# Kernel tuning notes

Hardware: AMD Instinct MI355X
Metric: run time of the kernel (lower is better)

## Reference

```python
import jax, jax.numpy as jnp
import numpy as np

B, N, D = 8, 4096, 512
NUM_CODES = 8192

def setup_inputs() -> dict:
    key = jax.random.key(0)
    kx, kc = jax.random.split(key)
    x = jax.random.normal(kx, (B, N, D), dtype=jnp.float32)
    codebook = jax.random.normal(kc, (NUM_CODES, D), dtype=jnp.float32)
    return {"x": x, "codebook": codebook}

def reference(x, codebook):
    # x: (B, N, D); codebook: (K, D)
    b = x.shape[0]
    flat = x.reshape(-1, x.shape[-1])  # (B*N, D)
    distances = (
        jnp.sum(flat * flat, axis=1, keepdims=True)
        + jnp.sum(codebook * codebook, axis=1)
        - 2.0 * flat @ codebook.T
    )
    codes = jnp.argmin(distances, axis=1).reshape(b, -1)  # (B, N) int
    return codes
```

## Files before the change

### kernel.cpp

```cpp
#include <hip/hip_runtime.h>
#include <hip/hip_bf16.h>
#include <hip/hip_fp16.h>


#define M_ROWS 32768
#define DDIM   512
#define KCODES 8192
#define NCAND  8

typedef unsigned long long u64;
typedef unsigned int u32;
typedef __attribute__((ext_vector_type(4))) float f32x4;
typedef __attribute__((ext_vector_type(2))) long l64x2;

#define GL2LDS(gp, lp) __builtin_amdgcn_global_load_lds(                  \
    (const __attribute__((address_space(1))) void*)(gp),                  \
    (__attribute__((address_space(3))) void*)(lp), 16, 0, 0)

__device__ __forceinline__ u32 umin32(u32 a, u32 b) { return a < b ? a : b; }
__device__ __forceinline__ u32 umax32(u32 a, u32 b) { return a > b ? a : b; }
__device__ __forceinline__ u64 umin64(u64 a, u64 b) { return a < b ? a : b; }

__device__ __forceinline__ u32 fsort(float s) {
  u32 fb = __float_as_uint(s);
  return fb ^ (u32)(((int)fb >> 31) | 0x80000000);
}

__device__ __forceinline__ uint2 pk8_fp8(float4 v0, float4 v1) {
  int lo = 0, hi = 0;
  lo = __builtin_amdgcn_cvt_pk_fp8_f32(v0.x, v0.y, lo, false);
  lo = __builtin_amdgcn_cvt_pk_fp8_f32(v0.z, v0.w, lo, true);
  hi = __builtin_amdgcn_cvt_pk_fp8_f32(v1.x, v1.y, hi, false);
  hi = __builtin_amdgcn_cvt_pk_fp8_f32(v1.z, v1.w, hi, true);
  return (uint2){(u32)lo, (u32)hi};
}

__device__ __forceinline__ size_t frag_addr(int row, int lane8 ) {
  const int c  = lane8 >> 4;
  const int k16 = lane8 & 15;
  const int ks = k16 >> 2;
  const int g  = k16 & 3;
  const int q  = g * 2 + (ks >> 1);
  const int slot = q ^ (row & 7);
  return (size_t)row * 512 + c * 128 + slot * 16 + (ks & 1) * 8;
}

__global__ __launch_bounds__(256) void conv_codebook_kernel(
    const float* __restrict__ cb, unsigned char* __restrict__ ch8,
    float* __restrict__ cnh) {
  int wave = (blockIdx.x * 256 + threadIdx.x) >> 6;
  int lane = threadIdx.x & 63;
  if (wave >= KCODES) return;
  const float* src = cb + (size_t)wave * DDIM + lane * 8;
  float4 v0 = *(const float4*)(src);
  float4 v1 = *(const float4*)(src + 4);
  *(uint2*)(ch8 + frag_addr(wave, lane)) = pk8_fp8(v0, v1);
  float ss = v0.x*v0.x + v0.y*v0.y + v0.z*v0.z + v0.w*v0.w
           + v1.x*v1.x + v1.y*v1.y + v1.z*v1.z + v1.w*v1.w;
#pragma unroll
  for (int off = 32; off; off >>= 1) ss += __shfl_xor(ss, off);
  if (lane == 0) cnh[wave] = 0.5f * ss;
}

__global__ __launch_bounds__(256) void conv_x_kernel(
    const float* __restrict__ x, unsigned char* __restrict__ xh8) {
  int wave = (blockIdx.x * 256 + threadIdx.x) >> 6;
  int lane = threadIdx.x & 63;
  const float* src = x + (size_t)wave * DDIM + lane * 8;
  float4 v0 = *(const float4*)(src);
  float4 v1 = *(const float4*)(src + 4);
  *(uint2*)(xh8 + frag_addr(wave, lane)) = pk8_fp8(v0, v1);
}

__global__ __launch_bounds__(256) void coarse_kernel(
    const unsigned char* __restrict__ xh8, const unsigned char* __restrict__ ch8,
    const float* __restrict__ cnh, uint4* __restrict__ part) {
  __shared__ __align__(16) char smem[34816];
  char* aL = smem;
  char* bL = smem + 16384;
  uint4* tab = (uint4*)smem;

  const int tid  = threadIdx.x;
  const int lane = tid & 63;
  const int wid  = tid >> 6;
  const int wm   = wid >> 1, wn = wid & 1;
  const int g    = lane >> 4, l16 = lane & 15;

  const int mblk = blockIdx.x & 255;
  const int nblk = blockIdx.x >> 8;
  const int row0 = mblk * 128;
  const int col0 = nblk * 128;

  const int a_ = lane >> 3, b_ = lane & 7;
  const int slot0 = (g * 2) ^ (l16 & 7);

  f32x4 acc[4][4];
#pragma unroll
  for (int tm = 0; tm < 4; ++tm)
#pragma unroll
    for (int tn = 0; tn < 4; ++tn) acc[tm][tn] = (f32x4){0.f, 0.f, 0.f, 0.f};

  for (int c = 0; c < 4; ++c) {
    __syncthreads();
#pragma unroll
    for (int j = 0; j < 4; ++j) {
      const int I = wid * 4 + j;
      const size_t srcoff = (size_t)(I * 8 + a_) * 512 + c * 128 + b_ * 16;
      GL2LDS(xh8 + (size_t)row0 * 512 + srcoff, aL + I * 1024);
      GL2LDS(ch8 + (size_t)col0 * 512 + srcoff, bL + I * 1024);
    }
    __syncthreads();
#pragma unroll
    for (int ks2 = 0; ks2 < 2; ++ks2) {
      const int slot = slot0 ^ ks2;
      l64x2 af[4], bf[4];
#pragma unroll
      for (int t = 0; t < 4; ++t) {
        const int ra = wm * 64 + t * 16 + l16;
        const int rb = wn * 64 + t * 16 + l16;
        af[t] = *(const l64x2*)&aL[ra * 128 + slot * 16];
        bf[t] = *(const l64x2*)&bL[rb * 128 + slot * 16];
      }
#pragma unroll
      for (int h = 0; h < 2; ++h)
#pragma unroll
        for (int tm = 0; tm < 4; ++tm)
#pragma unroll
          for (int tn = 0; tn < 4; ++tn)
            acc[tm][tn] = __builtin_amdgcn_mfma_f32_16x16x32_fp8_fp8(
                af[tm][h], bf[tn][h], acc[tm][tn], 0, 0, 0);
    }
  }

  u32 codev[4];
  float cn[4];
#pragma unroll
  for (int tn = 0; tn < 4; ++tn) {
    codev[tn] = (u32)(col0 + wn * 64 + tn * 16 + l16);
    cn[tn] = cnh[codev[tn]];
  }

  u32 k1[16], k2[16], k3[16];
#pragma unroll
  for (int tm = 0; tm < 4; ++tm)
#pragma unroll
    for (int r = 0; r < 4; ++r) {
      const int sl = tm * 4 + r;
      k1[sl] = ~0u; k2[sl] = ~0u; k3[sl] = ~0u;
#pragma unroll
      for (int tn = 0; tn < 4; ++tn) {
        float s = cn[tn] - acc[tm][tn][r];
        u32 key = (__float_as_uint(s) & 0xFFFFE000u) | codev[tn];
        u32 t1 = umax32(k1[sl], key); k1[sl] = umin32(k1[sl], key);
        u32 t2 = umax32(k2[sl], t1);  k2[sl] = umin32(k2[sl], t1);
        k3[sl] = umin32(k3[sl], t2);
      }
    }

  u32 m1 = ~0u, m2 = ~0u, m3 = ~0u;
#pragma unroll
  for (int p = 0; p < 2; ++p) {
    __syncthreads();
    if (wn == p) {
#pragma unroll
      for (int tm = 0; tm < 4; ++tm)
#pragma unroll
        for (int r = 0; r < 4; ++r) {
          const int row = wm * 64 + tm * 16 + g * 4 + r;
          const int sl = tm * 4 + r;
          tab[row * 17 + l16] = (uint4){k1[sl], k2[sl], k3[sl], 0u};
        }
    }
    __syncthreads();
    if (tid < 128) {
#pragma unroll
      for (int e = 0; e < 16; ++e) {
        uint4 v = tab[tid * 17 + e];
        u32 t1 = umax32(m1, v.x); m1 = umin32(m1, v.x);
        u32 t2 = umax32(m2, t1);  m2 = umin32(m2, t1);
        m3 = umin32(m3, t2);
        t1 = umax32(m2, v.y);     m2 = umin32(m2, v.y);
        m3 = umin32(m3, t1);
        m3 = umin32(m3, v.z);
      }
    }
  }

  if (tid < 128)
    part[(size_t)nblk * M_ROWS + row0 + tid] = (uint4){m1, m2, m3, 0u};
}

__global__ __launch_bounds__(256) void merge_kernel(
    const uint4* __restrict__ part, int* __restrict__ cand) {
  const int row = blockIdx.x * 256 + threadIdx.x;
  u32 k[NCAND];
#pragma unroll
  for (int i = 0; i < NCAND; ++i) k[i] = ~0u;
  for (int nb = 0; nb < KCODES / 128; ++nb) {
    uint4 e = part[(size_t)nb * M_ROWS + row];
    u32 t = e.x;
#pragma unroll
    for (int i = 0; i < NCAND; ++i) { u32 mx = umax32(k[i], t); k[i] = umin32(k[i], t); t = mx; }
    t = e.y;
#pragma unroll
    for (int i = 0; i < NCAND; ++i) { u32 mx = umax32(k[i], t); k[i] = umin32(k[i], t); t = mx; }
    t = e.z;
#pragma unroll
    for (int i = 0; i < NCAND; ++i) { u32 mx = umax32(k[i], t); k[i] = umin32(k[i], t); t = mx; }
  }
#pragma unroll
  for (int i = 0; i < NCAND; ++i)
    cand[row * NCAND + i] = (int)(k[i] & 0x1FFFu);
}

__global__ __launch_bounds__(256) void rescore_kernel(
    const float* __restrict__ x, const float* __restrict__ cb,
    const float* __restrict__ cnh, const int* __restrict__ cand,
    int* __restrict__ out) {
  int wave = (blockIdx.x * 256 + threadIdx.x) >> 6;
  int lane = threadIdx.x & 63;
  if (wave >= M_ROWS) return;
  int idx[NCAND];
#pragma unroll
  for (int j = 0; j < NCAND; ++j) idx[j] = cand[wave * NCAND + j];

  const float* xr = x + (size_t)wave * DDIM + lane * 8;
  float4 x0 = *(const float4*)(xr);
  float4 x1 = *(const float4*)(xr + 4);

  float d[NCAND];
#pragma unroll
  for (int j = 0; j < NCAND; ++j) {
    const float* c = cb + (size_t)idx[j] * DDIM + lane * 8;
    float4 a0 = *(const float4*)(c);
    float4 a1 = *(const float4*)(c + 4);
    d[j] = x0.x*a0.x + x0.y*a0.y + x0.z*a0.z + x0.w*a0.w
         + x1.x*a1.x + x1.y*a1.y + x1.z*a1.z + x1.w*a1.w;
  }
#pragma unroll
  for (int off = 32; off; off >>= 1)
#pragma unroll
    for (int j = 0; j < NCAND; ++j) d[j] += __shfl_xor(d[j], off);

  if (lane == 0) {
    u64 best = ~0ull;
#pragma unroll
    for (int j = 0; j < NCAND; ++j) {
      float s = cnh[idx[j]] - d[j];
      u64 key = ((u64)fsort(s) << 32) | (u32)idx[j];
      best = umin64(best, key);
    }
    out[wave] = (int)(u32)best;
  }
}

extern "C" void kernel_launch(void* const* d_in, const int* in_sizes, int n_in,
                              void* d_out, int out_size, void* d_ws, size_t ws_size,
                              hipStream_t stream) {
  const float* x  = (const float*)d_in[0];
  const float* cb = (const float*)d_in[1];
  int* out = (int*)d_out;

  char* ws = (char*)d_ws;
  unsigned char* ch8  = (unsigned char*)(ws);
  unsigned char* xh8  = (unsigned char*)(ws + (size_t)4 * 1024 * 1024);
  float*         cnh  = (float*)(ws + (size_t)20 * 1024 * 1024);
  int*           cand = (int*)(ws + (size_t)20 * 1024 * 1024 + 32 * 1024);
  uint4*         part = (uint4*)(ws + (size_t)21 * 1024 * 1024);

  conv_codebook_kernel<<<KCODES / 4, 256, 0, stream>>>(cb, ch8, cnh);
  conv_x_kernel<<<M_ROWS / 4, 256, 0, stream>>>(x, xh8);
  coarse_kernel<<<(M_ROWS / 128) * (KCODES / 128), 256, 0, stream>>>(xh8, ch8, cnh, part);
  merge_kernel<<<M_ROWS / 256, 256, 0, stream>>>(part, cand);
  rescore_kernel<<<M_ROWS / 4, 256, 0, stream>>>(x, cb, cnh, cand, out);
}
```

Measured before the change: 403.3 us.

## Switch coarse GEMM to gfx950 16x16x128 scaled FP8 MFMA with row-major layout

Replaces the 16x16x32 FP8 MFMA sequence with the gfx950 mfma_scale 16x16x128 f8f6f4 instruction using unit scales (0x7F), so each K-chunk of 128 takes one MFMA per tile instead of four. The FP8 conversion kernels now write plain row-major data, and the XOR swizzle moves into the global-to-LDS copy addresses. Fragments are read from LDS as two 16-byte pieces per lane. The part buffer offset is also moved. The risk is that the new fragment K-ordering must match for both A and B, which is fine for a dot product, and the wider operands raise register pressure.

Result: faster. 383.5 us (-4.9%).

```diff
diff --git a/kernel.cpp b/kernel.cpp
--- a/kernel.cpp
+++ b/kernel.cpp
@@ -11,7 +11,7 @@
 typedef unsigned long long u64;
 typedef unsigned int u32;
 typedef __attribute__((ext_vector_type(4))) float f32x4;
-typedef __attribute__((ext_vector_type(2))) long l64x2;
+typedef __attribute__((ext_vector_type(8))) int v8i;
 
 #define GL2LDS(gp, lp) __builtin_amdgcn_global_load_lds(                  \
     (const __attribute__((address_space(1))) void*)(gp),                  \
@@ -33,16 +33,6 @@
   hi = __builtin_amdgcn_cvt_pk_fp8_f32(v1.x, v1.y, hi, false);
   hi = __builtin_amdgcn_cvt_pk_fp8_f32(v1.z, v1.w, hi, true);
   return (uint2){(u32)lo, (u32)hi};
-}
-
-__device__ __forceinline__ size_t frag_addr(int row, int lane8 ) {
-  const int c  = lane8 >> 4;
-  const int k16 = lane8 & 15;
-  const int ks = k16 >> 2;
-  const int g  = k16 & 3;
-  const int q  = g * 2 + (ks >> 1);
-  const int slot = q ^ (row & 7);
-  return (size_t)row * 512 + c * 128 + slot * 16 + (ks & 1) * 8;
 }
 
 __global__ __launch_bounds__(256) void conv_codebook_kernel(
@@ -54,7 +44,7 @@
   const float* src = cb + (size_t)wave * DDIM + lane * 8;
   float4 v0 = *(const float4*)(src);
   float4 v1 = *(const float4*)(src + 4);
-  *(uint2*)(ch8 + frag_addr(wave, lane)) = pk8_fp8(v0, v1);
+  *(uint2*)(ch8 + (size_t)wave * DDIM + lane * 8) = pk8_fp8(v0, v1);
   float ss = v0.x*v0.x + v0.y*v0.y + v0.z*v0.z + v0.w*v0.w
            + v1.x*v1.x + v1.y*v1.y + v1.z*v1.z + v1.w*v1.w;
 #pragma unroll
@@ -64,12 +54,21 @@
 
 __global__ __launch_bounds__(256) void conv_x_kernel(
     const float* __restrict__ x, unsigned char* __restrict__ xh8) {
-  int wave = (blockIdx.x * 256 + threadIdx.x) >> 6;
-  int lane = threadIdx.x & 63;
-  const float* src = x + (size_t)wave * DDIM + lane * 8;
-  float4 v0 = *(const float4*)(src);
-  float4 v1 = *(const float4*)(src + 4);
-  *(uint2*)(xh8 + frag_addr(wave, lane)) = pk8_fp8(v0, v1);
+  size_t i = ((size_t)blockIdx.x * 256 + threadIdx.x) * 8;
+  float4 v0 = *(const float4*)(x + i);
+  float4 v1 = *(const float4*)(x + i + 4);
+  *(uint2*)(xh8 + i) = pk8_fp8(v0, v1);
+}
+
+__device__ __forceinline__ v8i ld_frag(const char* L, int row, int g) {
+  const int base = row * 128;
+  const int sl = ((g * 2) ^ (row & 7)) * 16;
+  int4 lo = *(const int4*)&L[base + sl];
+  int4 hi = *(const int4*)&L[base + (sl ^ 16)];
+  v8i r;
+  r[0] = lo.x; r[1] = lo.y; r[2] = lo.z; r[3] = lo.w;
+  r[4] = hi.x; r[5] = hi.y; r[6] = hi.z; r[7] = hi.w;
+  return r;
 }
 
 __global__ __launch_bounds__(256) void coarse_kernel(
@@ -92,7 +91,7 @@
   const int col0 = nblk * 128;
 
   const int a_ = lane >> 3, b_ = lane & 7;
-  const int slot0 = (g * 2) ^ (l16 & 7);
+  const size_t gsrc = (size_t)a_ * DDIM + ((b_ ^ a_) << 4);
 
   f32x4 acc[4][4];
 #pragma unroll
@@ -100,35 +99,32 @@
 #pragma unroll
     for (int tn = 0; tn < 4; ++tn) acc[tm][tn] = (f32x4){0.f, 0.f, 0.f, 0.f};
 
+#pragma unroll
   for (int c = 0; c < 4; ++c) {
     __syncthreads();
 #pragma unroll
     for (int j = 0; j < 4; ++j) {
       const int I = wid * 4 + j;
-      const size_t srcoff = (size_t)(I * 8 + a_) * 512 + c * 128 + b_ * 16;
-      GL2LDS(xh8 + (size_t)row0 * 512 + srcoff, aL + I * 1024);
-      GL2LDS(ch8 + (size_t)col0 * 512 + srcoff, bL + I * 1024);
-    }
-    __syncthreads();
-#pragma unroll
-    for (int ks2 = 0; ks2 < 2; ++ks2) {
-      const int slot = slot0 ^ ks2;
-      l64x2 af[4], bf[4];
-#pragma unroll
-      for (int t = 0; t < 4; ++t) {
-        const int ra = wm * 64 + t * 16 + l16;
-        const int rb = wn * 64 + t * 16 + l16;
-        af[t] = *(const l64x2*)&aL[ra * 128 + slot * 16];
-        bf[t] = *(const l64x2*)&bL[rb * 128 + slot * 16];
-      }
-#pragma unroll
-      for (int h = 0; h < 2; ++h)
-#pragma unroll
-        for (int tm = 0; tm < 4; ++tm)
-#pragma unroll
-          for (int tn = 0; tn < 4; ++tn)
-            acc[tm][tn] = __builtin_amdgcn_mfma_f32_16x16x32_fp8_fp8(
-                af[tm][h], bf[tn][h], acc[tm][tn], 0, 0, 0);
+      const size_t off = (size_t)(I * 8) * DDIM + c * 128 + gsrc;
+      GL2LDS(xh8 + (size_t)row0 * DDIM + off, aL + I * 1024);
+      GL2LDS(ch8 + (size_t)col0 * DDIM + off, bL + I * 1024);
+    }
+    __syncthreads();
+
+    v8i af[4];
+#pragma unroll
+    for (int t = 0; t < 4; ++t)
+      af[t] = ld_frag(aL, wm * 64 + t * 16 + l16, g);
+#pragma unroll
+    for (int tn = 0; tn < 4; ++tn) {
+      v8i bf = ld_frag(bL, wn * 64 + tn * 16 + l16, g);
+#pragma unroll
+      for (int tm = 0; tm < 4; ++tm)
+        acc[tm][tn] = __builtin_amdgcn_mfma_scale_f32_16x16x128_f8f6f4(
+            af[tm], bf, acc[tm][tn],
+            0, 0,
+            0, 0x7F7F7F7F,
+            0, 0x7F7F7F7F);
     }
   }
 
@@ -266,10 +262,10 @@
   unsigned char* xh8  = (unsigned char*)(ws + (size_t)4 * 1024 * 1024);
   float*         cnh  = (float*)(ws + (size_t)20 * 1024 * 1024);
   int*           cand = (int*)(ws + (size_t)20 * 1024 * 1024 + 32 * 1024);
-  uint4*         part = (uint4*)(ws + (size_t)21 * 1024 * 1024);
+  uint4*         part = (uint4*)(ws + (size_t)22 * 1024 * 1024);
 
   conv_codebook_kernel<<<KCODES / 4, 256, 0, stream>>>(cb, ch8, cnh);
-  conv_x_kernel<<<M_ROWS / 4, 256, 0, stream>>>(x, xh8);
+  conv_x_kernel<<<(M_ROWS * DDIM) / (256 * 8), 256, 0, stream>>>(x, xh8);
   coarse_kernel<<<(M_ROWS / 128) * (KCODES / 128), 256, 0, stream>>>(xh8, ch8, cnh, part);
   merge_kernel<<<M_ROWS / 256, 256, 0, stream>>>(part, cand);
   rescore_kernel<<<M_ROWS / 4, 256, 0, stream>>>(x, cb, cnh, cand, out);
```
